# Optimization experiments

Hardware: AMD Instinct MI355X
Metric: run time of the kernel (lower is better)

The kernel has to match this reference:

```python
import jax, jax.numpy as jnp
import numpy as np

N_ENT, N_REL, D, H, N_MID = 4096, 200, 128, 4, 9  # 1 input layer + 9 middle layers + 1 out layer
ALPHA = 0.2
NEG = -9e15


def gat_head(x, adj_mask, W, a):
    # x: [N, Fin], W: [Fin, Fout], a: [2*Fout]
    Wh = x @ W                                   # [N, Fout]
    d = Wh.shape[-1]
    f1 = Wh @ a[:d]                              # [N]
    f2 = Wh @ a[d:]                              # [N]
    e = jax.nn.leaky_relu(f1[:, None] + f2[None, :], ALPHA)  # [N, N]
    e = jnp.where(adj_mask, e, NEG)
    attn = jax.nn.softmax(e, axis=-1)
    return attn @ Wh                             # [N, Fout]


def multihead_concat(x, adj_mask, Ws, As):
    # Ws: [H, Fin, Fout], As: [H, 2*Fout] -> elu(concat over heads) [N, H*Fout]
    heads = jax.vmap(lambda W, a: gat_head(x, adj_mask, W, a))(Ws, As)  # [H, N, Fout]
    N = x.shape[0]
    return jax.nn.elu(jnp.transpose(heads, (1, 0, 2)).reshape(N, -1))


def setup_inputs() -> dict:
    key = jax.random.key(0)
    ks = jax.random.split(key, 12)
    s = 0.1
    return {
        "head": jax.random.randint(ks[0], (4096,), 0, N_ENT),
        "relation": jax.random.randint(ks[1], (4096,), 0, N_REL),
        "adj": jax.random.normal(ks[2], (N_ENT, N_ENT), dtype=jnp.float32),
        "entity_emb": jax.random.normal(ks[3], (N_ENT, D), dtype=jnp.float32) * s,
        "relation_emb": jax.random.normal(ks[4], (N_REL, D), dtype=jnp.float32) * s,
        "W0": jax.random.normal(ks[5], (H, D, D), dtype=jnp.float32) * s,
        "a0": jax.random.normal(ks[6], (H, 2 * D), dtype=jnp.float32) * s,
        "Wm": jax.random.normal(ks[7], (N_MID, H, H * D, D), dtype=jnp.float32) * s,
        "am": jax.random.normal(ks[8], (N_MID, H, 2 * D), dtype=jnp.float32) * s,
        "Wo": jax.random.normal(ks[9], (H * D, D), dtype=jnp.float32) * s,
        "ao": jax.random.normal(ks[10], (2 * D,), dtype=jnp.float32) * s,
    }


def reference(head, relation, adj, entity_emb, relation_emb, W0, a0, Wm, am, Wo, ao):
    adj_mask = adj > 0
    # layer 0: D -> H*D
    x = multihead_concat(entity_emb, adj_mask, W0, a0)
    # 9 middle layers: H*D -> H*D (identical shapes -> scan)
    def step(x, params):
        Ws, As = params
        return multihead_concat(x, adj_mask, Ws, As), None
    x, _ = jax.lax.scan(step, x, (Wm, am))
    # output layer: single head H*D -> D, elu applied after
    x = jax.nn.elu(gat_head(x, adj_mask, Wo, ao))
    head_relation_combined = entity_emb[head] + relation_emb[relation]
    return (x, head_relation_combined)
```

## Files before the change

kernel.cpp:

```cpp
#include <hip/hip_runtime.h>

typedef unsigned short u16;
typedef short bf16x8 __attribute__((ext_vector_type(8)));
typedef float f32x4 __attribute__((ext_vector_type(4)));

__device__ __forceinline__ float bf2f(unsigned v) { return __uint_as_float(v << 16); }
__device__ __forceinline__ u16 f2bf(float f) {
    unsigned u = __float_as_uint(f);
    return (u16)((u + 0x7fffu + ((u >> 16) & 1u)) >> 16);
}

__device__ __forceinline__ void gload_lds16(const void* g, void* l) {
    __builtin_amdgcn_global_load_lds(
        (const __attribute__((address_space(1))) unsigned int*)g,
        (__attribute__((address_space(3))) unsigned int*)l, 16, 0, 0);
}


__global__ __launch_bounds__(256) void k_mask(const float* __restrict__ adj,
                                              unsigned* __restrict__ mask) {
    int w = blockIdx.x * 256 + threadIdx.x;
    const float4* q = (const float4*)(adj + (size_t)w * 32);
    unsigned bits = 0u;
#pragma unroll
    for (int i = 0; i < 8; i++) {
        float4 v = q[i];
        if (v.x > 0.f) bits |= (1u << (i * 4 + 0));
        if (v.y > 0.f) bits |= (1u << (i * 4 + 1));
        if (v.z > 0.f) bits |= (1u << (i * 4 + 2));
        if (v.w > 0.f) bits |= (1u << (i * 4 + 3));
    }
    mask[w] = bits;
}

__global__ void k_trans(const float* __restrict__ in, u16* __restrict__ out, int K) {
    __shared__ float t[32][33];
    const float* src = in + (size_t)blockIdx.z * K * 128;
    u16* dst = out + (size_t)blockIdx.z * K * 128;
    int k0 = blockIdx.x * 32, n0 = blockIdx.y * 32;
    int tx = threadIdx.x, ty = threadIdx.y;
#pragma unroll
    for (int i = 0; i < 32; i += 8) t[ty + i][tx] = src[(size_t)(k0 + ty + i) * 128 + n0 + tx];
    __syncthreads();
#pragma unroll
    for (int i = 0; i < 32; i += 8) dst[(size_t)(n0 + ty + i) * K + k0 + tx] = f2bf(t[tx][ty + i]);
}

__global__ __launch_bounds__(256) void k_cvt(const float* __restrict__ in,
                                             u16* __restrict__ out) {
    int t = blockIdx.x * 256 + threadIdx.x;
    float4 v = ((const float4*)in)[t];
    uint2 o;
    o.x = (unsigned)f2bf(v.x) | ((unsigned)f2bf(v.y) << 16);
    o.y = (unsigned)f2bf(v.z) | ((unsigned)f2bf(v.w) << 16);
    ((uint2*)out)[t] = o;
}

__global__ __launch_bounds__(1024, 4) void k_proj(const u16* __restrict__ X,
                                                  const u16* __restrict__ WT,
                                                  const float* __restrict__ avec,
                                                  u16* __restrict__ WhT,
                                                  float* __restrict__ f1,
                                                  float* __restrict__ f2, int Fin) {
    __shared__ u16 As[2][64 * 32];
    __shared__ u16 Bs[2][128 * 32];
    __shared__ float fpart[4][64][2];
    const int tid = threadIdx.x;
    const int wv = tid >> 6, lane = tid & 63;
    const int rg = wv & 3, cg = wv >> 2;
    const int c = lane & 15, quad = lane >> 4;
    const int bofs = (quad ^ ((c >> 1) & 3)) * 8;
    const int h = blockIdx.y;
    const int j0 = blockIdx.x * 64;
    const u16* Wp = WT + (size_t)h * 128 * Fin;
    const int sgr = ((lane & 3) ^ ((lane >> 3) & 3)) * 8;

#define PROJ_STAGE(buf, kb)                                                              \
    do {                                                                                 \
        if (cg == 0)                                                                     \
            gload_lds16(X + (size_t)(j0 + rg * 16 + (lane >> 2)) * Fin + (kb) + sgr,     \
                        (void*)&As[buf][rg * 16 * 32]);                                  \
        else if (cg <= 2)                                                                \
            gload_lds16(Wp + (size_t)((cg - 1) * 64 + rg * 16 + (lane >> 2)) * Fin + (kb) + sgr, \
                        (void*)&Bs[buf][((cg - 1) * 64 + rg * 16) * 32]);                \
    } while (0)

    PROJ_STAGE(0, 0);
    __syncthreads();

    f32x4 acc[2];
    acc[0] = (f32x4){0.f, 0.f, 0.f, 0.f};
    acc[1] = (f32x4){0.f, 0.f, 0.f, 0.f};

    int it = 0;
    for (int kb = 0; kb < Fin; kb += 32, it++) {
        const int cur = it & 1;
        if (kb + 32 < Fin) PROJ_STAGE(cur ^ 1, kb + 32);
        bf16x8 av = *(const bf16x8*)&As[cur][(rg * 16 + c) * 32 + bofs];
#pragma unroll
        for (int e = 0; e < 2; e++) {
            bf16x8 bv = *(const bf16x8*)&Bs[cur][((cg * 2 + e) * 16 + c) * 32 + bofs];
            acc[e] = __builtin_amdgcn_mfma_f32_16x16x32_bf16(av, bv, acc[e], 0, 0, 0);
        }
        __syncthreads();
    }

    u16* Wo = WhT + (size_t)h * 128 * 4096;
    const float* ah = avec + h * 256;
    float p1[4] = {0, 0, 0, 0}, p2[4] = {0, 0, 0, 0};
#pragma unroll
    for (int e = 0; e < 2; e++) {
        const int n = (cg * 2 + e) * 16 + c;
        float a1 = ah[n];
        float a2 = ah[128 + n];
        u16 w4[4];
#pragma unroll
        for (int r = 0; r < 4; r++) {
            float v = acc[e][r];
            w4[r] = f2bf(v);
            p1[r] += v * a1;
            p2[r] += v * a2;
        }
        uint2 pk;
        pk.x = (unsigned)w4[0] | ((unsigned)w4[1] << 16);
        pk.y = (unsigned)w4[2] | ((unsigned)w4[3] << 16);
        *(uint2*)&Wo[(size_t)n * 4096 + j0 + rg * 16 + quad * 4] = pk;
    }
#pragma unroll
    for (int off = 1; off < 16; off <<= 1) {
#pragma unroll
        for (int r = 0; r < 4; r++) {
            p1[r] += __shfl_xor(p1[r], off);
            p2[r] += __shfl_xor(p2[r], off);
        }
    }
    if (c == 0) {
#pragma unroll
        for (int r = 0; r < 4; r++) {
            fpart[cg][rg * 16 + quad * 4 + r][0] = p1[r];
            fpart[cg][rg * 16 + quad * 4 + r][1] = p2[r];
        }
    }
    __syncthreads();
    if (tid < 64) {
        float s1 = fpart[0][tid][0] + fpart[1][tid][0] + fpart[2][tid][0] + fpart[3][tid][0];
        float s2 = fpart[0][tid][1] + fpart[1][tid][1] + fpart[2][tid][1] + fpart[3][tid][1];
        f1[h * 4096 + j0 + tid] = s1;
        f2[h * 4096 + j0 + tid] = s2;
    }
}

template <bool F32OUT>
__global__ __launch_bounds__(512, 2) void k_attn(const u16* __restrict__ WhT,
                                                 const float* __restrict__ f1g,
                                                 const float* __restrict__ f2g,
                                                 const unsigned char* __restrict__ maskb,
                                                 void* __restrict__ outp, int ostride) {
    __shared__ float f2s[4096];
    __shared__ unsigned char ms[64 * 528];
    __shared__ u16 Bs[2][4][128 * 32];
    __shared__ float f1s[64];
    __shared__ float lpart[4][64];
    __shared__ float redmax[8];
    __shared__ float red[64 * 132];

    const int tid = threadIdx.x;
    const int wv = tid >> 6, lane = tid & 63;
    const int jg = wv >> 1, rg = wv & 1;
    const int c = lane & 15, quad = lane >> 4;
    const int bofs = (quad ^ ((c >> 1) & 3)) * 8;
    const int sgr = ((lane & 3) ^ ((lane >> 3) & 3)) * 8;
    const int h = blockIdx.y;
    const int i0 = blockIdx.x * 64;
    const float LOG2E = 1.4426950408889634f;
    const float* f1h = f1g + h * 4096;
    const float* f2h = f2g + h * 4096;
    const u16* Wp = WhT + (size_t)h * 128 * 4096;

#define ATTN_STAGE(buf, kb)                                                              \
    do {                                                                                 \
        const int jb_ = jg * 1024 + (kb) * 32;                                           \
        _Pragma("unroll")                                                                \
        for (int e_ = 0; e_ < 4; e_++)                                                   \
            gload_lds16(Wp + (size_t)(rg * 64 + e_ * 16 + (lane >> 2)) * 4096 + jb_ + sgr, \
                        (void*)&Bs[buf][jg][(rg * 64 + e_ * 16) * 32]);                  \
    } while (0)

    float mymax = -3.0e38f;
#pragma unroll
    for (int e = 0; e < 2; e++) {
        float4 v = ((const float4*)f2h)[tid + e * 512];
        v.x *= LOG2E; v.y *= LOG2E; v.z *= LOG2E; v.w *= LOG2E;
        ((float4*)f2s)[tid + e * 512] = v;
        mymax = fmaxf(mymax, fmaxf(fmaxf(v.x, v.y), fmaxf(v.z, v.w)));
    }
    if (tid < 64) f1s[tid] = f1h[i0 + tid] * LOG2E;
    {
        const uint4* msrc = (const uint4*)(maskb + (size_t)i0 * 512);
#pragma unroll
        for (int e = 0; e < 4; e++) {
            int o = tid + e * 512;
            uint4 v = msrc[o];
            int row = o >> 5, col = o & 31;
            *(uint4*)&ms[row * 528 + col * 16] = v;
        }
    }
    ATTN_STAGE(0, 0);
#pragma unroll
    for (int off = 1; off < 64; off <<= 1) mymax = fmaxf(mymax, __shfl_xor(mymax, off));
    if (lane == 0) redmax[wv] = mymax;
    __syncthreads();
    float F2MAX = redmax[0];
#pragma unroll
    for (int i = 1; i < 8; i++) F2MAX = fmaxf(F2MAX, redmax[i]);

    const int iloc0 = rg * 32 + c;
    const int iloc1 = iloc0 + 16;
    const float rf1a = f1s[iloc0];
    const float rf1b = f1s[iloc1];
    const float za = rf1a + F2MAX, zb = rf1b + F2MAX;
    const float rma = fmaxf(za, 0.2f * za), rmb = fmaxf(zb, 0.2f * zb);
    const float Aca = rf1a - rma, Bca = 0.2f * rf1a - rma;
    const float Acb = rf1b - rmb, Bcb = 0.2f * rf1b - rmb;

    f32x4 acc[2][8];
#pragma unroll
    for (int f = 0; f < 2; f++)
#pragma unroll
        for (int i = 0; i < 8; i++) acc[f][i] = (f32x4){0.f, 0.f, 0.f, 0.f};
    float lsa = 0.f, lsb = 0.f;

    for (int kb = 0; kb < 32; kb++) {
        const int cur = kb & 1;
        if (kb < 31) ATTN_STAGE(cur ^ 1, kb + 1);
        const int jb = jg * 1024 + kb * 32;
        const int mofs = jg * 128 + kb * 4 + quad;
        const unsigned mba = ms[iloc0 * 528 + mofs];
        const unsigned mbb = ms[iloc1 * 528 + mofs];
        const float4 fa = *(const float4*)&f2s[jb + quad * 8];
        const float4 fb = *(const float4*)&f2s[jb + quad * 8 + 4];
        const float f2v[8] = {fa.x, fa.y, fa.z, fa.w, fb.x, fb.y, fb.z, fb.w};
        union { bf16x8 v; unsigned u[4]; } afa, afb;
#pragma unroll
        for (int t = 0; t < 8; t += 2) {
            float g0 = f2v[t], g1 = f2v[t + 1];
            float sa0 = fmaxf(Aca + g0, __builtin_fmaf(0.2f, g0, Bca));
            float sa1 = fmaxf(Aca + g1, __builtin_fmaf(0.2f, g1, Bca));
            float sb0 = fmaxf(Acb + g0, __builtin_fmaf(0.2f, g0, Bcb));
            float sb1 = fmaxf(Acb + g1, __builtin_fmaf(0.2f, g1, Bcb));
            float pa0 = __builtin_amdgcn_exp2f(sa0);
            float pa1 = __builtin_amdgcn_exp2f(sa1);
            float pb0 = __builtin_amdgcn_exp2f(sb0);
            float pb1 = __builtin_amdgcn_exp2f(sb1);
            unsigned ua0 = ((mba >> t) & 1u)       ? (__float_as_uint(pa0) & 0xffff0000u) : 0u;
            unsigned ua1 = ((mba >> (t + 1)) & 1u) ? (__float_as_uint(pa1) & 0xffff0000u) : 0u;
            unsigned ub0 = ((mbb >> t) & 1u)       ? (__float_as_uint(pb0) & 0xffff0000u) : 0u;
            unsigned ub1 = ((mbb >> (t + 1)) & 1u) ? (__float_as_uint(pb1) & 0xffff0000u) : 0u;
            lsa += __uint_as_float(ua0) + __uint_as_float(ua1);
            lsb += __uint_as_float(ub0) + __uint_as_float(ub1);
            afa.u[t >> 1] = (ua0 >> 16) | ua1;
            afb.u[t >> 1] = (ub0 >> 16) | ub1;
        }
#pragma unroll
        for (int nt = 0; nt < 8; nt++) {
            bf16x8 bv = *(const bf16x8*)&Bs[cur][jg][(nt * 16 + c) * 32 + bofs];
            acc[0][nt] = __builtin_amdgcn_mfma_f32_16x16x32_bf16(afa.v, bv, acc[0][nt], 0, 0, 0);
            acc[1][nt] = __builtin_amdgcn_mfma_f32_16x16x32_bf16(afb.v, bv, acc[1][nt], 0, 0, 0);
        }
        __syncthreads();
    }

    lsa += __shfl_xor(lsa, 16);
    lsa += __shfl_xor(lsa, 32);
    lsb += __shfl_xor(lsb, 16);
    lsb += __shfl_xor(lsb, 32);
    if (quad == 0) {
        lpart[jg][iloc0] = lsa;
        lpart[jg][iloc1] = lsb;
    }

#pragma unroll
    for (int g = 0; g < 4; g++) {
        __syncthreads();
        if (jg == g) {
#pragma unroll
            for (int f = 0; f < 2; f++) {
#pragma unroll
                for (int nt = 0; nt < 8; nt++) {
#pragma unroll
                    for (int r = 0; r < 4; r++) {
                        int idx = (rg * 32 + f * 16 + quad * 4 + r) * 132 + nt * 16 + c;
                        if (g == 0) red[idx] = acc[f][nt][r];
                        else        red[idx] += acc[f][nt][r];
                    }
                }
            }
        }
    }
    __syncthreads();

    const int row = tid >> 3, ob = tid & 7;
    const float l = lpart[0][row] + lpart[1][row] + lpart[2][row] + lpart[3][row];
    const float linv = 1.0f / l;
    float vv[16];
#pragma unroll
    for (int half = 0; half < 2; half++) {
#pragma unroll
        for (int t = 0; t < 8; t++) {
            float v = red[row * 132 + (ob + half * 8) * 8 + t] * linv;
            vv[half * 8 + t] = v > 0.f ? v : __expf(v) - 1.f;
        }
    }
    const size_t obase = (size_t)(i0 + row) * ostride + h * 128 + ob * 8;
    if (F32OUT) {
        float* op = (float*)outp + obase;
        *(float4*)op = *(float4*)&vv[0];
        *(float4*)(op + 4) = *(float4*)&vv[4];
        *(float4*)(op + 64) = *(float4*)&vv[8];
        *(float4*)(op + 68) = *(float4*)&vv[12];
    } else {
        u16* op = (u16*)outp + obase;
        uint4 o;
        o.x = (unsigned)f2bf(vv[0]) | ((unsigned)f2bf(vv[1]) << 16);
        o.y = (unsigned)f2bf(vv[2]) | ((unsigned)f2bf(vv[3]) << 16);
        o.z = (unsigned)f2bf(vv[4]) | ((unsigned)f2bf(vv[5]) << 16);
        o.w = (unsigned)f2bf(vv[6]) | ((unsigned)f2bf(vv[7]) << 16);
        *(uint4*)op = o;
        o.x = (unsigned)f2bf(vv[8])  | ((unsigned)f2bf(vv[9]) << 16);
        o.y = (unsigned)f2bf(vv[10]) | ((unsigned)f2bf(vv[11]) << 16);
        o.z = (unsigned)f2bf(vv[12]) | ((unsigned)f2bf(vv[13]) << 16);
        o.w = (unsigned)f2bf(vv[14]) | ((unsigned)f2bf(vv[15]) << 16);
        *(uint4*)(op + 64) = o;
    }
}

__global__ __launch_bounds__(256) void k_gather(const int* __restrict__ head,
                                                const int* __restrict__ rel,
                                                const float* __restrict__ ent,
                                                const float* __restrict__ rele,
                                                float* __restrict__ out) {
    int t = blockIdx.x * 256 + threadIdx.x;
    int row = t >> 5, sg = t & 31;
    int hh = head[row], rr = rel[row];
    float4 a = ((const float4*)(ent + (size_t)hh * 128))[sg];
    float4 b = ((const float4*)(rele + (size_t)rr * 128))[sg];
    float4 o;
    o.x = a.x + b.x; o.y = a.y + b.y; o.z = a.z + b.z; o.w = a.w + b.w;
    ((float4*)(out + (size_t)row * 128))[sg] = o;
}

extern "C" void kernel_launch(void* const* d_in, const int* in_sizes, int n_in,
                              void* d_out, int out_size, void* d_ws, size_t ws_size,
                              hipStream_t stream) {
    const int*   head = (const int*)d_in[0];
    const int*   rel  = (const int*)d_in[1];
    const float* adj  = (const float*)d_in[2];
    const float* ent  = (const float*)d_in[3];
    const float* rele = (const float*)d_in[4];
    const float* W0   = (const float*)d_in[5];
    const float* a0   = (const float*)d_in[6];
    const float* Wm   = (const float*)d_in[7];
    const float* am   = (const float*)d_in[8];
    const float* Wo   = (const float*)d_in[9];
    const float* ao   = (const float*)d_in[10];

    char* ws = (char*)d_ws;
    unsigned* mask = (unsigned*)(ws + 0);
    u16* WT0 = (u16*)(ws + 2097152);
    u16* WT5 = (u16*)(ws + 2228224);
    u16* WhT = (u16*)(ws + 7077888);
    float* f1 = (float*)(ws + 11272192);
    float* f2 = (float*)(ws + 11337728);
    u16* xA = (u16*)(ws + 11403264);
    u16* xB = (u16*)(ws + 15597568);
    u16* x0 = (u16*)(ws + 19791872);

    float* out_x = (float*)d_out;
    float* out_comb = out_x + (size_t)4096 * 128;

    k_mask<<<2048, 256, 0, stream>>>(adj, mask);
    k_cvt<<<512, 256, 0, stream>>>(ent, x0);
    k_trans<<<dim3(4, 4, 4), dim3(32, 8), 0, stream>>>(W0, WT0, 128);
    k_trans<<<dim3(16, 4, 36), dim3(32, 8), 0, stream>>>(Wm, WT5, 512);
    k_trans<<<dim3(16, 4, 1), dim3(32, 8), 0, stream>>>(Wo, WT5 + (size_t)36 * 512 * 128, 512);
    k_gather<<<512, 256, 0, stream>>>(head, rel, ent, rele, out_comb);

    k_proj<<<dim3(64, 4), 1024, 0, stream>>>(x0, WT0, a0, WhT, f1, f2, 128);
    k_attn<false><<<dim3(64, 4), 512, 0, stream>>>(WhT, f1, f2, (const unsigned char*)mask, xA, 512);
    u16 *xc = xA, *xn = xB;
    for (int l = 0; l < 9; l++) {
        k_proj<<<dim3(64, 4), 1024, 0, stream>>>(xc, WT5 + (size_t)l * 4 * 512 * 128,
                                                 am + (size_t)l * 4 * 256, WhT, f1, f2, 512);
        k_attn<false><<<dim3(64, 4), 512, 0, stream>>>(WhT, f1, f2, (const unsigned char*)mask, xn, 512);
        u16* t = xc; xc = xn; xn = t;
    }
    k_proj<<<dim3(64, 1), 1024, 0, stream>>>(xc, WT5 + (size_t)36 * 512 * 128, ao, WhT, f1, f2, 512);
    k_attn<true><<<dim3(64, 1), 512, 0, stream>>>(WhT, f1, f2, (const unsigned char*)mask, out_x, 128);
}
```

Baseline: 704.9 us.

## Factor attention exponentials into per-column tables and software-pipeline softmax with MFMA

The leaky-relu exponent is split into row and column factors. Each column's exp2 values are precomputed once into an LDS table, so the inner loop needs only a compare, a select and a multiply instead of an exp per element. Mask bits come from a 256-entry LUT of lane masks, the row sums are computed by an extra MFMA against a ones vector, and the mask bytes are read straight from global memory instead of being staged in LDS. The main loop is unrolled by two so that the probability computation for the next tile overlaps the MFMAs of the current one. The risks are reduced precision from multiplying exponentials that can underflow or overflow, and more register pressure.

Measured after the change: 838.8 us. 1.19x slower.

```diff
diff --git a/kernel.cpp b/kernel.cpp
--- a/kernel.cpp
+++ b/kernel.cpp
@@ -156,10 +156,9 @@
                                                  const float* __restrict__ f2g,
                                                  const unsigned char* __restrict__ maskb,
                                                  void* __restrict__ outp, int ostride) {
-    __shared__ float f2s[4096];
-    __shared__ unsigned char ms[64 * 528];
+    __shared__ float E12[8192];
+    __shared__ unsigned LUTM[256 * 8];
     __shared__ u16 Bs[2][4][128 * 32];
-    __shared__ float f1s[64];
     __shared__ float lpart[4][64];
     __shared__ float redmax[8];
     __shared__ float red[64 * 132];
@@ -186,26 +185,33 @@
                         (void*)&Bs[buf][jg][(rg * 64 + e_ * 16) * 32]);                  \
     } while (0)
 
+    float f2p[8];
     float mymax = -3.0e38f;
-#pragma unroll
-    for (int e = 0; e < 2; e++) {
-        float4 v = ((const float4*)f2h)[tid + e * 512];
-        v.x *= LOG2E; v.y *= LOG2E; v.z *= LOG2E; v.w *= LOG2E;
-        ((float4*)f2s)[tid + e * 512] = v;
-        mymax = fmaxf(mymax, fmaxf(fmaxf(v.x, v.y), fmaxf(v.z, v.w)));
-    }
-    if (tid < 64) f1s[tid] = f1h[i0 + tid] * LOG2E;
     {
-        const uint4* msrc = (const uint4*)(maskb + (size_t)i0 * 512);
-#pragma unroll
-        for (int e = 0; e < 4; e++) {
-            int o = tid + e * 512;
-            uint4 v = msrc[o];
-            int row = o >> 5, col = o & 31;
-            *(uint4*)&ms[row * 528 + col * 16] = v;
-        }
+        float4 v0 = ((const float4*)f2h)[tid * 2];
+        float4 v1 = ((const float4*)f2h)[tid * 2 + 1];
+        f2p[0] = v0.x * LOG2E; f2p[1] = v0.y * LOG2E;
+        f2p[2] = v0.z * LOG2E; f2p[3] = v0.w * LOG2E;
+        f2p[4] = v1.x * LOG2E; f2p[5] = v1.y * LOG2E;
+        f2p[6] = v1.z * LOG2E; f2p[7] = v1.w * LOG2E;
+#pragma unroll
+        for (int k = 0; k < 8; k++) mymax = fmaxf(mymax, f2p[k]);
+    }
+    if (tid < 256) {
+        uint4 a, b;
+        a.x = (tid & 1)   ? 0xffff0000u : 0u;
+        a.y = (tid & 2)   ? 0xffff0000u : 0u;
+        a.z = (tid & 4)   ? 0xffff0000u : 0u;
+        a.w = (tid & 8)   ? 0xffff0000u : 0u;
+        b.x = (tid & 16)  ? 0xffff0000u : 0u;
+        b.y = (tid & 32)  ? 0xffff0000u : 0u;
+        b.z = (tid & 64)  ? 0xffff0000u : 0u;
+        b.w = (tid & 128) ? 0xffff0000u : 0u;
+        *(uint4*)&LUTM[tid * 8] = a;
+        *(uint4*)&LUTM[tid * 8 + 4] = b;
     }
     ATTN_STAGE(0, 0);
+
 #pragma unroll
     for (int off = 1; off < 64; off <<= 1) mymax = fmaxf(mymax, __shfl_xor(mymax, off));
     if (lane == 0) redmax[wv] = mymax;
@@ -214,69 +220,117 @@
 #pragma unroll
     for (int i = 1; i < 8; i++) F2MAX = fmaxf(F2MAX, redmax[i]);
 
+    {
+        const int j0w = tid * 8;
+#pragma unroll
+        for (int k = 0; k < 8; k += 2) {
+            float d0 = f2p[k] - F2MAX, d1 = f2p[k + 1] - F2MAX;
+            float4 w;
+            w.x = __builtin_amdgcn_exp2f(d0);
+            w.y = __builtin_amdgcn_exp2f(0.2f * d0);
+            w.z = __builtin_amdgcn_exp2f(d1);
+            w.w = __builtin_amdgcn_exp2f(0.2f * d1);
+            *(float4*)&E12[2 * (j0w + k)] = w;
+        }
+    }
+
     const int iloc0 = rg * 32 + c;
     const int iloc1 = iloc0 + 16;
-    const float rf1a = f1s[iloc0];
-    const float rf1b = f1s[iloc1];
+    const float rf1a = f1h[i0 + iloc0] * LOG2E;
+    const float rf1b = f1h[i0 + iloc1] * LOG2E;
     const float za = rf1a + F2MAX, zb = rf1b + F2MAX;
     const float rma = fmaxf(za, 0.2f * za), rmb = fmaxf(zb, 0.2f * zb);
-    const float Aca = rf1a - rma, Bca = 0.2f * rf1a - rma;
-    const float Acb = rf1b - rmb, Bcb = 0.2f * rf1b - rmb;
+    const float C1a = __builtin_amdgcn_exp2f(za - rma);
+    const float C2a = __builtin_amdgcn_exp2f(0.2f * za - rma);
+    const float Ta  = __builtin_amdgcn_exp2f(-za);
+    const float C1b = __builtin_amdgcn_exp2f(zb - rmb);
+    const float C2b = __builtin_amdgcn_exp2f(0.2f * zb - rmb);
+    const float Tb  = __builtin_amdgcn_exp2f(-zb);
+
+    const unsigned char* mpa = maskb + (size_t)(i0 + iloc0) * 512 + jg * 128 + quad;
+    const unsigned char* mpb = maskb + (size_t)(i0 + iloc1) * 512 + jg * 128 + quad;
+    unsigned mA0 = mpa[0], mB0 = mpb[0];
+    unsigned mA1 = mpa[4], mB1 = mpb[4];
+
+    bf16x8 onesv;
+#pragma unroll
+    for (int i = 0; i < 8; i++) onesv[i] = (short)0x3F80;
 
     f32x4 acc[2][8];
 #pragma unroll
     for (int f = 0; f < 2; f++)
 #pragma unroll
         for (int i = 0; i < 8; i++) acc[f][i] = (f32x4){0.f, 0.f, 0.f, 0.f};
-    float lsa = 0.f, lsb = 0.f;
-
-    for (int kb = 0; kb < 32; kb++) {
-        const int cur = kb & 1;
-        if (kb < 31) ATTN_STAGE(cur ^ 1, kb + 1);
-        const int jb = jg * 1024 + kb * 32;
-        const int mofs = jg * 128 + kb * 4 + quad;
-        const unsigned mba = ms[iloc0 * 528 + mofs];
-        const unsigned mbb = ms[iloc1 * 528 + mofs];
-        const float4 fa = *(const float4*)&f2s[jb + quad * 8];
-        const float4 fb = *(const float4*)&f2s[jb + quad * 8 + 4];
-        const float f2v[8] = {fa.x, fa.y, fa.z, fa.w, fb.x, fb.y, fb.z, fb.w};
-        union { bf16x8 v; unsigned u[4]; } afa, afb;
-#pragma unroll
-        for (int t = 0; t < 8; t += 2) {
-            float g0 = f2v[t], g1 = f2v[t + 1];
-            float sa0 = fmaxf(Aca + g0, __builtin_fmaf(0.2f, g0, Bca));
-            float sa1 = fmaxf(Aca + g1, __builtin_fmaf(0.2f, g1, Bca));
-            float sb0 = fmaxf(Acb + g0, __builtin_fmaf(0.2f, g0, Bcb));
-            float sb1 = fmaxf(Acb + g1, __builtin_fmaf(0.2f, g1, Bcb));
-            float pa0 = __builtin_amdgcn_exp2f(sa0);
-            float pa1 = __builtin_amdgcn_exp2f(sa1);
-            float pb0 = __builtin_amdgcn_exp2f(sb0);
-            float pb1 = __builtin_amdgcn_exp2f(sb1);
-            unsigned ua0 = ((mba >> t) & 1u)       ? (__float_as_uint(pa0) & 0xffff0000u) : 0u;
-            unsigned ua1 = ((mba >> (t + 1)) & 1u) ? (__float_as_uint(pa1) & 0xffff0000u) : 0u;
-            unsigned ub0 = ((mbb >> t) & 1u)       ? (__float_as_uint(pb0) & 0xffff0000u) : 0u;
-            unsigned ub1 = ((mbb >> (t + 1)) & 1u) ? (__float_as_uint(pb1) & 0xffff0000u) : 0u;
-            lsa += __uint_as_float(ua0) + __uint_as_float(ua1);
-            lsb += __uint_as_float(ub0) + __uint_as_float(ub1);
-            afa.u[t >> 1] = (ua0 >> 16) | ua1;
-            afb.u[t >> 1] = (ub0 >> 16) | ub1;
-        }
-#pragma unroll
-        for (int nt = 0; nt < 8; nt++) {
-            bf16x8 bv = *(const bf16x8*)&Bs[cur][jg][(nt * 16 + c) * 32 + bofs];
-            acc[0][nt] = __builtin_amdgcn_mfma_f32_16x16x32_bf16(afa.v, bv, acc[0][nt], 0, 0, 0);
-            acc[1][nt] = __builtin_amdgcn_mfma_f32_16x16x32_bf16(afb.v, bv, acc[1][nt], 0, 0, 0);
-        }
+    f32x4 acc_l[2];
+    acc_l[0] = (f32x4){0.f, 0.f, 0.f, 0.f};
+    acc_l[1] = (f32x4){0.f, 0.f, 0.f, 0.f};
+
+    union AF { bf16x8 v; unsigned u[4]; };
+    AF af0a, af0b, af1a, af1b;
+
+#define COMP_P(dstA, dstB, kb, mba_, mbb_)                                               \
+    do {                                                                                 \
+        const int jc_ = jg * 1024 + (kb) * 32 + quad * 8;                                \
+        const unsigned* LA_ = &LUTM[(mba_) * 8];                                         \
+        const unsigned* LB_ = &LUTM[(mbb_) * 8];                                         \
+        uint4 Ma0_ = *(const uint4*)LA_;  uint4 Ma1_ = *(const uint4*)(LA_ + 4);         \
+        uint4 Mb0_ = *(const uint4*)LB_;  uint4 Mb1_ = *(const uint4*)(LB_ + 4);         \
+        const unsigned MA_[8] = {Ma0_.x, Ma0_.y, Ma0_.z, Ma0_.w,                         \
+                                 Ma1_.x, Ma1_.y, Ma1_.z, Ma1_.w};                        \
+        const unsigned MB_[8] = {Mb0_.x, Mb0_.y, Mb0_.z, Mb0_.w,                         \
+                                 Mb1_.x, Mb1_.y, Mb1_.z, Mb1_.w};                        \
+        _Pragma("unroll")                                                                \
+        for (int t = 0; t < 8; t += 2) {                                                 \
+            float4 e_ = *(const float4*)&E12[2 * (jc_ + t)];                             \
+            float pa0 = ((e_.x > Ta) ? C1a : C2a) * ((e_.x > Ta) ? e_.x : e_.y);         \
+            float pa1 = ((e_.z > Ta) ? C1a : C2a) * ((e_.z > Ta) ? e_.z : e_.w);         \
+            float pb0 = ((e_.x > Tb) ? C1b : C2b) * ((e_.x > Tb) ? e_.x : e_.y);         \
+            float pb1 = ((e_.z > Tb) ? C1b : C2b) * ((e_.z > Tb) ? e_.z : e_.w);         \
+            unsigned ua0 = __float_as_uint(pa0) & MA_[t];                                \
+            unsigned ua1 = __float_as_uint(pa1) & MA_[t + 1];                            \
+            unsigned ub0 = __float_as_uint(pb0) & MB_[t];                                \
+            unsigned ub1 = __float_as_uint(pb1) & MB_[t + 1];                            \
+            dstA.u[t >> 1] = (ua0 >> 16) | ua1;                                          \
+            dstB.u[t >> 1] = (ub0 >> 16) | ub1;                                          \
+        }                                                                                \
+    } while (0)
+
+#define DO_MFMA(srcA, srcB, buf)                                                         \
+    do {                                                                                 \
+        _Pragma("unroll")                                                                \
+        for (int nt = 0; nt < 8; nt++) {                                                 \
+            bf16x8 bv_ = *(const bf16x8*)&Bs[buf][jg][(nt * 16 + c) * 32 + bofs];        \
+            acc[0][nt] = __builtin_amdgcn_mfma_f32_16x16x32_bf16(srcA.v, bv_, acc[0][nt], 0, 0, 0); \
+            acc[1][nt] = __builtin_amdgcn_mfma_f32_16x16x32_bf16(srcB.v, bv_, acc[1][nt], 0, 0, 0); \
+        }                                                                                \
+        acc_l[0] = __builtin_amdgcn_mfma_f32_16x16x32_bf16(srcA.v, onesv, acc_l[0], 0, 0, 0); \
+        acc_l[1] = __builtin_amdgcn_mfma_f32_16x16x32_bf16(srcB.v, onesv, acc_l[1], 0, 0, 0); \
+    } while (0)
+
+    __syncthreads();
+    COMP_P(af0a, af0b, 0, mA0, mB0);
+
+    for (int kb = 0; kb < 32; kb += 2) {
+        ATTN_STAGE(1, kb + 1);
+        if (kb + 2 < 32) { mA0 = mpa[4 * (kb + 2)]; mB0 = mpb[4 * (kb + 2)]; }
+        COMP_P(af1a, af1b, kb + 1, mA1, mB1);
+        DO_MFMA(af0a, af0b, 0);
         __syncthreads();
-    }
-
-    lsa += __shfl_xor(lsa, 16);
-    lsa += __shfl_xor(lsa, 32);
-    lsb += __shfl_xor(lsb, 16);
-    lsb += __shfl_xor(lsb, 32);
-    if (quad == 0) {
-        lpart[jg][iloc0] = lsa;
-        lpart[jg][iloc1] = lsb;
+        if (kb < 30) {
+            ATTN_STAGE(0, kb + 2);
+            if (kb + 3 < 32) { mA1 = mpa[4 * (kb + 3)]; mB1 = mpb[4 * (kb + 3)]; }
+            COMP_P(af0a, af0b, kb + 2, mA0, mB0);
+        }
+        DO_MFMA(af1a, af1b, 1);
+        __syncthreads();
+    }
+
+    if (c == 0) {
+#pragma unroll
+        for (int f = 0; f < 2; f++)
+#pragma unroll
+            for (int r = 0; r < 4; r++)
+                lpart[jg][rg * 32 + f * 16 + quad * 4 + r] = acc_l[f][r];
     }
 
 #pragma unroll
```
